# Optimization experiments

Measured on AMD Instinct MI355X. Metric: run time of the kernel, lower is better.

## Reference

```python
import jax, jax.numpy as jnp
import numpy as np
import math

NUM_REF = 8
STD = 5.0
B, D = 8192, 512


def setup_inputs() -> dict:
    key = jax.random.key(0)
    k1, k2 = jax.random.split(key)
    Struct = jax.random.normal(k1, (B, D), dtype=jnp.float32)
    Label = jax.random.uniform(k2, (B,), dtype=jnp.float32)
    return {"Struct": Struct, "Label": Label}


def reference(Struct, Label):
    # Pairwise |label_j - label_i| : [B, B]
    res_abs = jnp.abs(Label[None, :] - Label[:, None])
    # Num_ref nearest labels per sample (torch.sort ascending + take first K)
    _, idx = jax.lax.top_k(-res_abs, NUM_REF)          # [B, K]
    Struct_ref = Struct[idx]                            # [B, K, D]
    Label_ref = jax.lax.stop_gradient(Label[idx])       # [B, K] (detached)
    mean = Label[:, None]                               # [B, 1]
    # Gaussian smoothing weights, normalized over the K refs
    w = jnp.exp(-(Label_ref - mean) ** 2 / (2.0 * STD ** 2)) / (
        jnp.sqrt(jnp.asarray(2.0 * math.pi, Struct.dtype)) * STD)
    w = w / jnp.sum(w, axis=1, keepdims=True)           # [B, K]
    Struct_mean = jnp.einsum("bk,bkd->bd", w, Struct_ref)  # [B, D]
    # cosine similarity between Struct and Struct_mean, averaged over batch
    l1 = Struct / (1e-10 + jnp.linalg.norm(Struct, axis=1, keepdims=True))
    l2 = Struct_mean / (1e-10 + jnp.linalg.norm(Struct_mean, axis=1, keepdims=True))
    sim = jnp.mean(jnp.sum(l1 * l2, axis=1))
    return 1.0 - sim
```

## Files before the change

kernel.cpp:

```cpp
#include <hip/hip_runtime.h>
#include <math.h>

#define BN 8192
#define DN 512
#define KN 8
#define WIN 8

typedef unsigned long long u64;
typedef unsigned int u32;

#define OFF_KEYS  0
#define OFF_PART  65536

__device__ __forceinline__ u32 flip_f32(u32 f) {
  return f ^ (u32)(((int)f >> 31) | 0x80000000);
}
__device__ __forceinline__ float unflip_f32(u32 f) {
  return __uint_as_float((f & 0x80000000u) ? (f ^ 0x80000000u) : ~f);
}

__device__ __forceinline__ u64 shfl_xor_u64(u64 v, int mask) {
  u32 lo = (u32)v, hi = (u32)(v >> 32);
  lo = (u32)__shfl_xor((int)lo, mask, 64);
  hi = (u32)__shfl_xor((int)hi, mask, 64);
  return ((u64)hi << 32) | lo;
}
__device__ __forceinline__ u64 shfl_u64(u64 v, int src) {
  u32 lo = (u32)v, hi = (u32)(v >> 32);
  lo = (u32)__shfl((int)lo, src, 64);
  hi = (u32)__shfl((int)hi, src, 64);
  return ((u64)hi << 32) | lo;
}

__global__ __launch_bounds__(256) void ranksort_kernel(const float* __restrict__ L,
                                                       u64* __restrict__ keys_out) {
  __shared__ u64 kk[BN];
  const int tid  = threadIdx.x;
  const int lane = tid & 63;
  const int wv   = tid >> 6;

#pragma unroll
  for (int t = 0; t < BN / 256; t++) {
    const int i = tid + t * 256;
    kk[i] = ((u64)flip_f32(__float_as_uint(L[i])) << 32) | (u32)i;
  }
  __syncthreads();

  const int wave_g = blockIdx.x * 4 + wv;
  const int e0 = wave_g * 4;
  const u64 k0 = kk[e0 + 0];
  const u64 k1 = kk[e0 + 1];
  const u64 k2 = kk[e0 + 2];
  const u64 k3 = kk[e0 + 3];

  int c0 = 0, c1 = 0, c2 = 0, c3 = 0;
#pragma unroll 4
  for (int t = lane; t < BN; t += 64) {
    const u64 v = kk[t];
    c0 += (v < k0); c1 += (v < k1); c2 += (v < k2); c3 += (v < k3);
  }
#pragma unroll
  for (int off = 1; off < 64; off <<= 1) {
    c0 += __shfl_xor(c0, off, 64);
    c1 += __shfl_xor(c1, off, 64);
    c2 += __shfl_xor(c2, off, 64);
    c3 += __shfl_xor(c3, off, 64);
  }
  if (lane == 0) {
    keys_out[c0] = k0;
    keys_out[c1] = k1;
    keys_out[c2] = k2;
    keys_out[c3] = k3;
  }
}

__global__ __launch_bounds__(256) void wmean_cos_kernel(const float* __restrict__ S,
                                                        const u64* __restrict__ keys,
                                                        float* __restrict__ partials) {
  const int tid  = threadIdx.x;
  const int lane = tid & 63;
  const int wv   = tid >> 6;
  const int blk  = blockIdx.x;
  const int xcd  = blk & 7;
  const int span = blk >> 3;
  const int rr   = xcd * 1024 + span * 4 + wv;

  const int q = rr - WIN + lane;
  const bool inw = (lane <= 2 * WIN) && (q >= 0) && (q < BN);
  const u64 wk = inw ? keys[q] : ~0ull;

  const u64 ckey = shfl_u64(wk, WIN);
  const float Lb = unflip_f32((u32)(ckey >> 32));
  const int   b  = (int)(u32)ckey;

  u64 key = ~0ull;
  if (wk != ~0ull) {
    const float lab = unflip_f32((u32)(wk >> 32));
    const float dist = fabsf(lab - Lb);
    key = ((u64)__float_as_uint(dist) << 32) | (u32)wk;
  }

#pragma unroll
  for (int k = 2; k <= 32; k <<= 1) {
#pragma unroll
    for (int j = 16; j > 0; j >>= 1) {
      if (j >= k) continue;
      const u64 o = shfl_xor_u64(key, j);
      const bool lower = (lane & j) == 0;
      const bool up = (lane & k) == 0;
      key = (up == lower) ? (key < o ? key : o) : (key < o ? o : key);
    }
  }

  float e = 0.0f;
  if (lane < 8) {
    const float d = __uint_as_float((u32)(key >> 32));
    e = expf(-d * d * (1.0f / 50.0f));
  }
  float ssum = e;
  ssum += __shfl_xor(ssum, 1, 64);
  ssum += __shfl_xor(ssum, 2, 64);
  ssum += __shfl_xor(ssum, 4, 64);
  const float wn = e / ssum;

  int ix[KN]; float w[KN];
  const int myidx = (int)(u32)key;
#pragma unroll
  for (int k = 0; k < KN; k++) {
    ix[k] = __shfl(myidx, k, 64);
    w[k]  = __shfl(wn,    k, 64);
  }

  const float4* Srow = (const float4*)(S + (size_t)b * DN);
  const float4 s0 = Srow[lane];
  const float4 s1 = Srow[lane + 64];

  float4 m0 = make_float4(0.f, 0.f, 0.f, 0.f);
  float4 m1 = make_float4(0.f, 0.f, 0.f, 0.f);
#pragma unroll
  for (int k = 0; k < KN; k++) {
    const float4* Nrow = (const float4*)(S + (size_t)ix[k] * DN);
    const float4 n0 = Nrow[lane];
    const float4 n1 = Nrow[lane + 64];
    const float wk2 = w[k];
    m0.x = fmaf(wk2, n0.x, m0.x); m0.y = fmaf(wk2, n0.y, m0.y);
    m0.z = fmaf(wk2, n0.z, m0.z); m0.w = fmaf(wk2, n0.w, m0.w);
    m1.x = fmaf(wk2, n1.x, m1.x); m1.y = fmaf(wk2, n1.y, m1.y);
    m1.z = fmaf(wk2, n1.z, m1.z); m1.w = fmaf(wk2, n1.w, m1.w);
  }

  float dot = s0.x * m0.x + s0.y * m0.y + s0.z * m0.z + s0.w * m0.w
            + s1.x * m1.x + s1.y * m1.y + s1.z * m1.z + s1.w * m1.w;
  float ns  = s0.x * s0.x + s0.y * s0.y + s0.z * s0.z + s0.w * s0.w
            + s1.x * s1.x + s1.y * s1.y + s1.z * s1.z + s1.w * s1.w;
  float nm  = m0.x * m0.x + m0.y * m0.y + m0.z * m0.z + m0.w * m0.w
            + m1.x * m1.x + m1.y * m1.y + m1.z * m1.z + m1.w * m1.w;

#pragma unroll
  for (int off = 32; off > 0; off >>= 1) {
    dot += __shfl_down(dot, off, 64);
    ns  += __shfl_down(ns,  off, 64);
    nm  += __shfl_down(nm,  off, 64);
  }

  __shared__ float psim[4];
  if (lane == 0) {
    psim[wv] = dot / ((1e-10f + sqrtf(ns)) * (1e-10f + sqrtf(nm)));
  }
  __syncthreads();
  if (tid == 0) {
    partials[blk] = psim[0] + psim[1] + psim[2] + psim[3];
  }
}

__global__ __launch_bounds__(256) void finalize_kernel(const float* __restrict__ partials,
                                                       float* __restrict__ out) {
  const int tid = threadIdx.x;
  float s = 0.0f;
  for (int i = tid; i < 2048; i += 256) s += partials[i];
#pragma unroll
  for (int off = 32; off > 0; off >>= 1) s += __shfl_down(s, off, 64);
  __shared__ float ps[4];
  if ((tid & 63) == 0) ps[tid >> 6] = s;
  __syncthreads();
  if (tid == 0) {
    const float tot = ps[0] + ps[1] + ps[2] + ps[3];
    out[0] = 1.0f - tot * (1.0f / (float)BN);
  }
}

extern "C" void kernel_launch(void* const* d_in, const int* in_sizes, int n_in,
                              void* d_out, int out_size, void* d_ws, size_t ws_size,
                              hipStream_t stream) {
  const float* S = (const float*)d_in[0];
  const float* L = (const float*)d_in[1];
  float* out = (float*)d_out;

  char* ws = (char*)d_ws;
  u64*   keys     = (u64*)  (ws + OFF_KEYS);
  float* partials = (float*)(ws + OFF_PART);

  ranksort_kernel<<<512, 256, 0, stream>>>(L, keys);
  wmean_cos_kernel<<<2048, 256, 0, stream>>>(S, keys, partials);
  finalize_kernel <<<1, 256, 0, stream>>>(partials, out);
}
```

Before: 80.29 us.

## Prefetch Struct into L2 during ranksort and hoist neighbor row loads

The rank-sort kernel now reads the whole Struct matrix (16 rows per block) into registers that it never uses, kept alive with empty asm. The point is to pull the 16 MB matrix into cache while the sort's compute-bound phase runs. The weighted-mean kernel issues the own-row and all eight neighbor-row loads before the exp and weight shuffles, so memory latency overlaps that work. It also gets a launch-bounds occupancy hint. The costs are extra register pressure in both kernels and the risk that the warmed data does not survive in the MI355X cache hierarchy until the second kernel runs.

```diff
diff --git a/kernel.cpp b/kernel.cpp
--- a/kernel.cpp
+++ b/kernel.cpp
@@ -33,11 +33,17 @@
 }
 
 __global__ __launch_bounds__(256) void ranksort_kernel(const float* __restrict__ L,
+                                                       const float* __restrict__ S,
                                                        u64* __restrict__ keys_out) {
   __shared__ u64 kk[BN];
   const int tid  = threadIdx.x;
   const int lane = tid & 63;
   const int wv   = tid >> 6;
+
+  const float4* Sw = (const float4*)(S + (size_t)blockIdx.x * 16 * DN);
+  float4 pre[8];
+#pragma unroll
+  for (int j = 0; j < 8; j++) pre[j] = Sw[tid + j * 256];
 
 #pragma unroll
   for (int t = 0; t < BN / 256; t++) {
@@ -72,11 +78,16 @@
     keys_out[c2] = k2;
     keys_out[c3] = k3;
   }
-}
-
-__global__ __launch_bounds__(256) void wmean_cos_kernel(const float* __restrict__ S,
-                                                        const u64* __restrict__ keys,
-                                                        float* __restrict__ partials) {
+
+#pragma unroll
+  for (int j = 0; j < 8; j++) {
+    asm volatile("" :: "v"(pre[j].x), "v"(pre[j].y), "v"(pre[j].z), "v"(pre[j].w));
+  }
+}
+
+__global__ __launch_bounds__(256, 4) void wmean_cos_kernel(const float* __restrict__ S,
+                                                           const u64* __restrict__ keys,
+                                                           float* __restrict__ partials) {
   const int tid  = threadIdx.x;
   const int lane = tid & 63;
   const int wv   = tid >> 6;
@@ -93,6 +104,10 @@
   const float Lb = unflip_f32((u32)(ckey >> 32));
   const int   b  = (int)(u32)ckey;
 
+  const float4* Srow = (const float4*)(S + (size_t)b * DN);
+  const float4 s0 = Srow[lane];
+  const float4 s1 = Srow[lane + 64];
+
   u64 key = ~0ull;
   if (wk != ~0ull) {
     const float lab = unflip_f32((u32)(wk >> 32));
@@ -112,6 +127,19 @@
     }
   }
 
+  const int myidx = (int)(u32)key;
+  int ix[KN];
+#pragma unroll
+  for (int k = 0; k < KN; k++) ix[k] = __shfl(myidx, k, 64);
+
+  float4 nb0[KN], nb1[KN];
+#pragma unroll
+  for (int k = 0; k < KN; k++) {
+    const float4* Nrow = (const float4*)(S + (size_t)ix[k] * DN);
+    nb0[k] = Nrow[lane];
+    nb1[k] = Nrow[lane + 64];
+  }
+
   float e = 0.0f;
   if (lane < 8) {
     const float d = __uint_as_float((u32)(key >> 32));
@@ -123,30 +151,19 @@
   ssum += __shfl_xor(ssum, 4, 64);
   const float wn = e / ssum;
 
-  int ix[KN]; float w[KN];
-  const int myidx = (int)(u32)key;
-#pragma unroll
-  for (int k = 0; k < KN; k++) {
-    ix[k] = __shfl(myidx, k, 64);
-    w[k]  = __shfl(wn,    k, 64);
-  }
-
-  const float4* Srow = (const float4*)(S + (size_t)b * DN);
-  const float4 s0 = Srow[lane];
-  const float4 s1 = Srow[lane + 64];
+  float w[KN];
+#pragma unroll
+  for (int k = 0; k < KN; k++) w[k] = __shfl(wn, k, 64);
 
   float4 m0 = make_float4(0.f, 0.f, 0.f, 0.f);
   float4 m1 = make_float4(0.f, 0.f, 0.f, 0.f);
 #pragma unroll
   for (int k = 0; k < KN; k++) {
-    const float4* Nrow = (const float4*)(S + (size_t)ix[k] * DN);
-    const float4 n0 = Nrow[lane];
-    const float4 n1 = Nrow[lane + 64];
     const float wk2 = w[k];
-    m0.x = fmaf(wk2, n0.x, m0.x); m0.y = fmaf(wk2, n0.y, m0.y);
-    m0.z = fmaf(wk2, n0.z, m0.z); m0.w = fmaf(wk2, n0.w, m0.w);
-    m1.x = fmaf(wk2, n1.x, m1.x); m1.y = fmaf(wk2, n1.y, m1.y);
-    m1.z = fmaf(wk2, n1.z, m1.z); m1.w = fmaf(wk2, n1.w, m1.w);
+    m0.x = fmaf(wk2, nb0[k].x, m0.x); m0.y = fmaf(wk2, nb0[k].y, m0.y);
+    m0.z = fmaf(wk2, nb0[k].z, m0.z); m0.w = fmaf(wk2, nb0[k].w, m0.w);
+    m1.x = fmaf(wk2, nb1[k].x, m1.x); m1.y = fmaf(wk2, nb1[k].y, m1.y);
+    m1.z = fmaf(wk2, nb1[k].z, m1.z); m1.w = fmaf(wk2, nb1[k].w, m1.w);
   }
 
   float dot = s0.x * m0.x + s0.y * m0.y + s0.z * m0.z + s0.w * m0.w
@@ -200,7 +217,7 @@
   u64*   keys     = (u64*)  (ws + OFF_KEYS);
   float* partials = (float*)(ws + OFF_PART);
 
-  ranksort_kernel<<<512, 256, 0, stream>>>(L, keys);
+  ranksort_kernel<<<512, 256, 0, stream>>>(L, S, keys);
   wmean_cos_kernel<<<2048, 256, 0, stream>>>(S, keys, partials);
   finalize_kernel <<<1, 256, 0, stream>>>(partials, out);
 }
```

After: 83.53 us. +4.0%, slower.
